# Kernel optimization log

Measured on AMD Instinct MI355X. Metric: run time of the kernel, lower is better.

The kernel has to match this reference:

```python
import jax, jax.numpy as jnp
import numpy as np

B, S, D = 2, 2048, 1024
N_HEADS, D_HEAD = 16, 64
INIT_STD = 0.02


def setup_inputs() -> dict:
    key = jax.random.key(0)
    k_res, k_q, k_k, k_v, k_o = jax.random.split(key, 5)
    residual = jax.random.normal(k_res, (B, S, D), dtype=jnp.float32)
    W_Q = INIT_STD * jax.random.normal(k_q, (N_HEADS, D_HEAD, D), dtype=jnp.float32)
    W_K = INIT_STD * jax.random.normal(k_k, (N_HEADS, D_HEAD, D), dtype=jnp.float32)
    W_V = INIT_STD * jax.random.normal(k_v, (N_HEADS, D_HEAD, D), dtype=jnp.float32)
    W_O = INIT_STD * jax.random.normal(k_o, (N_HEADS, D_HEAD, D), dtype=jnp.float32)
    return {"residual": residual, "W_Q": W_Q, "W_K": W_K, "W_V": W_V, "W_O": W_O}


def reference(residual, W_Q, W_K, W_V, W_O):
    seq_len = residual.shape[1]
    # projections: [b, n, p, h]  (heads first, matching q.transpose(1,2))
    q = jnp.einsum('bpd,nhd->bnph', residual, W_Q)
    k = jnp.einsum('bpd,nhd->bnph', residual, W_K)
    v = jnp.einsum('bpd,nhd->bnph', residual, W_V)
    scale = 1.0 / jnp.sqrt(jnp.asarray(q.shape[-1], dtype=residual.dtype))
    # [b, n, p_q, p_k] full score matrix (faithful to original naive impl)
    scores = jnp.einsum('bnqh,bnkh->bnqk', q, k) * scale
    causal = jnp.tril(jnp.ones((seq_len, seq_len), dtype=bool))
    scores = jnp.where(causal, scores, -jnp.inf)
    pattern = jax.nn.softmax(scores, axis=-1)
    attn_out = jnp.einsum('bnqk,bnkh->bnqh', pattern, v)
    # output projection summed over heads: 'bpnh,nhd->bpd'
    return jnp.einsum('bnph,nhd->bpd', attn_out, W_O)
```

## Files before the change

### kernel.cpp

```cpp
#include <hip/hip_runtime.h>
#include <math.h>


#define SS_ 2048
#define DD_ 1024
#define NH_ 16
#define BN_ 32
#define BS_ 4096

typedef __bf16 bf16x8 __attribute__((ext_vector_type(8)));
typedef __bf16 bf16x4 __attribute__((ext_vector_type(4)));
typedef short shortx4 __attribute__((ext_vector_type(4)));
typedef float floatx4 __attribute__((ext_vector_type(4)));
typedef unsigned short ushortx4 __attribute__((ext_vector_type(4)));

__device__ __forceinline__ unsigned short f2bf(float f) {
    union { float f; unsigned u; } v; v.f = f;
    unsigned r = v.u + 0x7FFFu + ((v.u >> 16) & 1u);
    return (unsigned short)(r >> 16);
}

__device__ __forceinline__ floatx4 mfma_pv(bf16x4 a, bf16x4 b, floatx4 c) {
#if __has_builtin(__builtin_amdgcn_mfma_f32_16x16x16_bf16)
    return __builtin_amdgcn_mfma_f32_16x16x16_bf16(a, b, c, 0, 0, 0);
#else
    return __builtin_amdgcn_mfma_f32_16x16x16bf16_1k(
        __builtin_bit_cast(shortx4, a), __builtin_bit_cast(shortx4, b), c, 0, 0, 0);
#endif
}

__device__ __forceinline__ void gl_lds16(const unsigned short* g, unsigned short* l) {
    __builtin_amdgcn_global_load_lds(
        (const __attribute__((address_space(1))) unsigned int*)g,
        (__attribute__((address_space(3))) unsigned int*)l, 16, 0, 0);
}

__global__ __launch_bounds__(256) void cast_bf16_kernel(
    const float* __restrict__ resid, const float* __restrict__ WQ,
    const float* __restrict__ WK, const float* __restrict__ WV,
    unsigned short* __restrict__ residB, unsigned short* __restrict__ WQb,
    unsigned short* __restrict__ WKb, unsigned short* __restrict__ WVb)
{
    const int z = blockIdx.y;
    if (z > 0 && blockIdx.x >= 1024) return;
    const float* src = (z == 0) ? resid : (z == 1) ? WQ : (z == 2) ? WK : WV;
    unsigned short* dst = (z == 0) ? residB : (z == 1) ? WQb : (z == 2) ? WKb : WVb;
    const int i = (blockIdx.x * 256 + threadIdx.x) * 4;
    float4 f = *(const float4*)(src + i);
    ushortx4 o;
    o[0] = f2bf(f.x); o[1] = f2bf(f.y); o[2] = f2bf(f.z); o[3] = f2bf(f.w);
    *(ushortx4*)(dst + i) = o;
}

__global__ __launch_bounds__(256) void wo_transpose_kernel(
    const float* __restrict__ WO, unsigned short* __restrict__ WOt)
{
    __shared__ float t[64][65];
    const int kk0 = blockIdx.x * 64, d0 = blockIdx.y * 64;
    #pragma unroll
    for (int it = 0; it < 16; ++it) {
        int idx = it * 256 + threadIdx.x;
        int r = idx >> 6, c = idx & 63;
        t[r][c] = WO[(kk0 + r) * DD_ + d0 + c];
    }
    __syncthreads();
    #pragma unroll
    for (int it = 0; it < 16; ++it) {
        int idx = it * 256 + threadIdx.x;
        int r = idx >> 6, c = idx & 63;
        WOt[(d0 + r) * DD_ + kk0 + c] = f2bf(t[c][r]);
    }
}

__global__ __launch_bounds__(256) void qkv_m97_kernel(
    const unsigned short* __restrict__ residB,
    const unsigned short* __restrict__ WQb,
    const unsigned short* __restrict__ WKb,
    const unsigned short* __restrict__ WVb,
    unsigned short* __restrict__ q, unsigned short* __restrict__ kk,
    unsigned short* __restrict__ vT)
{
    __shared__ unsigned short As[128 * 64];
    __shared__ unsigned short Bs[128 * 64];
    const int tid = threadIdx.x;
    const int l = tid & 63, w = tid >> 6;
    const int quad = l >> 4, lan = l & 15;
    const int z = blockIdx.z;
    const unsigned short* W = (z == 0) ? WQb : (z == 1) ? WKb : WVb;
    unsigned short* dst = (z == 0) ? q : (z == 1) ? kk : vT;
    const int mBase = blockIdx.x * 128;
    const int nBase = blockIdx.y * 128;
    const int wm = (w & 1) * 64, wn = (w >> 1) * 64;

    floatx4 acc[4][4];
    #pragma unroll
    for (int a = 0; a < 4; ++a)
        #pragma unroll
        for (int b = 0; b < 4; ++b)
            #pragma unroll
            for (int i = 0; i < 4; ++i) acc[a][b][i] = 0.f;

    const int sr = l >> 3;
    const int sgx = ((l & 7) ^ sr) * 8;
    const int sw = (l & 7) ^ (lan & 7);

    for (int k0 = 0; k0 < DD_; k0 += 64) {
        __syncthreads();
        #pragma unroll
        for (int i = 0; i < 4; ++i) {
            const int row = i * 32 + w * 8 + sr;
            gl_lds16(residB + (size_t)(mBase + row) * DD_ + k0 + sgx,
                     As + i * 2048 + w * 512);
            gl_lds16(W + (size_t)(nBase + row) * DD_ + k0 + sgx,
                     Bs + i * 2048 + w * 512);
        }
        __syncthreads();
        #pragma unroll
        for (int ks = 0; ks < 2; ++ks) {
            const int fo = (((ks * 4 + quad) ^ (lan & 7)) << 3);
            bf16x8 a[4], b[4];
            #pragma unroll
            for (int mi = 0; mi < 4; ++mi)
                a[mi] = *(const bf16x8*)(As + (wm + mi * 16 + lan) * 64 + fo);
            #pragma unroll
            for (int ni = 0; ni < 4; ++ni)
                b[ni] = *(const bf16x8*)(Bs + (wn + ni * 16 + lan) * 64 + fo);
            #pragma unroll
            for (int mi = 0; mi < 4; ++mi)
                #pragma unroll
                for (int ni = 0; ni < 4; ++ni)
                    acc[mi][ni] = __builtin_amdgcn_mfma_f32_16x16x32_bf16(
                        a[mi], b[ni], acc[mi][ni], 0, 0, 0);
        }
    }
    const int headU = (nBase + wn) >> 6;
    const float scale = (z == 0) ? 0.125f * 1.44269504088896340736f : 1.0f;
    if (z < 2) {
        #pragma unroll
        for (int mi = 0; mi < 4; ++mi)
            #pragma unroll
            for (int ni = 0; ni < 4; ++ni)
                #pragma unroll
                for (int reg = 0; reg < 4; ++reg) {
                    int m = mBase + wm + mi * 16 + quad * 4 + reg;
                    int bb = m >> 11, ss = m & 2047;
                    int h = ni * 16 + lan;
                    dst[((size_t)(bb * NH_ + headU) * SS_ + ss) * 64 + h] =
                        f2bf(acc[mi][ni][reg] * scale);
                }
    } else {
        #pragma unroll
        for (int mi = 0; mi < 4; ++mi) {
            const int m0 = mBase + wm + mi * 16 + quad * 4;
            const int bb = m0 >> 11, ss0 = m0 & 2047;
            #pragma unroll
            for (int ni = 0; ni < 4; ++ni) {
                const int h = ni * 16 + lan;
                bf16x4 ob;
                #pragma unroll
                for (int reg = 0; reg < 4; ++reg)
                    ob[reg] = static_cast<__bf16>(acc[mi][ni][reg]);
                *(bf16x4*)(dst + ((size_t)(bb * NH_ + headU) * 64 + h) * SS_ + ss0) = ob;
            }
        }
    }
}

__global__ __launch_bounds__(256) void flash_mfma_kernel(
    const unsigned short* __restrict__ q,
    const unsigned short* __restrict__ k,
    const unsigned short* __restrict__ vT,
    unsigned short* __restrict__ attn)
{
    __shared__ unsigned short ldsK[2][64 * 64];
    __shared__ unsigned short ldsV[2][64 * 64];
    const int l = threadIdx.x & 63, w = threadIdx.x >> 6;
    const int quad = l >> 4, lan = l & 15;
    const int f = blockIdx.x;
    const int bn = (f & 7) | (((f >> 3) & 3) << 3);
    const int p = f >> 5;

    const unsigned short* Qg = q  + (size_t)bn * SS_ * 64;
    const unsigned short* Kg = k  + (size_t)bn * SS_ * 64;
    const unsigned short* Vg = vT + (size_t)bn * 64 * SS_;

    const int srl = l >> 3;
    const int sgx = (l & 7) ^ srl;

    #pragma unroll
    for (int half = 0; half < 2; ++half) {
        const int chunk = (half == 0) ? p : 31 - p;
        const int qRow0 = chunk * 64 + w * 16;
        const int qAbs = qRow0 + lan;

        const unsigned short* Qr = Qg + (size_t)qAbs * 64 + quad * 8;
        bf16x8 Qf0 = *(const bf16x8*)(Qr);
        bf16x8 Qf1 = *(const bf16x8*)(Qr + 32);

        float mrow = -INFINITY, lrow = 0.f;
        floatx4 o[4];
        #pragma unroll
        for (int t = 0; t < 4; ++t)
            #pragma unroll
            for (int i = 0; i < 4; ++i) o[t][i] = 0.f;

        __syncthreads();
        #pragma unroll
        for (int i = 0; i < 2; ++i) {
            const int row = w * 16 + i * 8;
            gl_lds16(Kg + (size_t)(row + srl) * 64 + sgx * 8, &ldsK[0][row * 64]);
            gl_lds16(Vg + (size_t)(row + srl) * SS_ + sgx * 8, &ldsV[0][row * 64]);
        }

        for (int kt = 0; kt <= chunk; ++kt) {
            const int kBase = kt * 64;
            const int buf = kt & 1;
            __syncthreads();
            if (kt < chunk) {
                const int kB1 = kBase + 64;
                #pragma unroll
                for (int i = 0; i < 2; ++i) {
                    const int row = w * 16 + i * 8;
                    gl_lds16(Kg + (size_t)(kB1 + row + srl) * 64 + sgx * 8,
                             &ldsK[buf ^ 1][row * 64]);
                    gl_lds16(Vg + (size_t)(row + srl) * SS_ + kB1 + sgx * 8,
                             &ldsV[buf ^ 1][row * 64]);
                }
            }
            const unsigned short* Kb = &ldsK[buf][0];
            const unsigned short* Vb = &ldsV[buf][0];

            floatx4 sc[4];
            #pragma unroll
            for (int nt = 0; nt < 4; ++nt) {
                const unsigned short* kr = Kb + (nt * 16 + lan) * 64;
                bf16x8 K0 = *(const bf16x8*)(kr + ((quad ^ (lan & 7)) << 3));
                bf16x8 K1 = *(const bf16x8*)(kr + (((quad + 4) ^ (lan & 7)) << 3));
                floatx4 zz; zz[0] = zz[1] = zz[2] = zz[3] = 0.f;
                sc[nt] = __builtin_amdgcn_mfma_f32_16x16x32_bf16(K0, Qf0, zz, 0, 0, 0);
                sc[nt] = __builtin_amdgcn_mfma_f32_16x16x32_bf16(K1, Qf1, sc[nt], 0, 0, 0);
            }
            if (kt == chunk) {
                #pragma unroll
                for (int nt = 0; nt < 4; ++nt)
                    #pragma unroll
                    for (int reg = 0; reg < 4; ++reg)
                        if (kBase + nt * 16 + quad * 4 + reg > qAbs)
                            sc[nt][reg] = -INFINITY;
            }
            float mx = sc[0][0];
            #pragma unroll
            for (int nt = 0; nt < 4; ++nt)
                #pragma unroll
                for (int reg = 0; reg < 4; ++reg) mx = fmaxf(mx, sc[nt][reg]);
            mx = fmaxf(mx, __shfl_xor(mx, 16, 64));
            mx = fmaxf(mx, __shfl_xor(mx, 32, 64));
            const float mnew = fmaxf(mrow, mx);
            const float alpha = exp2f(mrow - mnew);
            bf16x4 pb[4];
            float sum = 0.f;
            #pragma unroll
            for (int nt = 0; nt < 4; ++nt)
                #pragma unroll
                for (int reg = 0; reg < 4; ++reg) {
                    float pp = exp2f(sc[nt][reg] - mnew);
                    sum += pp;
                    pb[nt][reg] = static_cast<__bf16>(pp);
                }
            sum += __shfl_xor(sum, 16, 64);
            sum += __shfl_xor(sum, 32, 64);
            lrow = lrow * alpha + sum;
            mrow = mnew;
            #pragma unroll
            for (int t = 0; t < 4; ++t)
                #pragma unroll
                for (int i = 0; i < 4; ++i) o[t][i] *= alpha;
            #pragma unroll
            for (int t = 0; t < 4; ++t) {
                const unsigned short* vr = Vb + (t * 16 + lan) * 64 + ((quad & 1) << 2);
                #pragma unroll
                for (int nt = 0; nt < 4; ++nt) {
                    const int g = nt * 2 + (quad >> 1);
                    bf16x4 Vf = *(const bf16x4*)(vr + ((g ^ (lan & 7)) << 3));
                    o[t] = mfma_pv(Vf, pb[nt], o[t]);
                }
            }
        }
        const float rl = 1.f / lrow;
        #pragma unroll
        for (int t = 0; t < 4; ++t) {
            bf16x4 ob;
            #pragma unroll
            for (int reg = 0; reg < 4; ++reg)
                ob[reg] = static_cast<__bf16>(o[t][reg] * rl);
            *(bf16x4*)(attn + ((size_t)bn * SS_ + qAbs) * 64 + t * 16 + quad * 4) = ob;
        }
    }
}

__global__ __launch_bounds__(256) void out_m97_kernel(
    const unsigned short* __restrict__ attn,
    const unsigned short* __restrict__ WOt,
    float* __restrict__ out)
{
    __shared__ unsigned short As[128 * 64];
    __shared__ unsigned short Bs[128 * 64];
    const int tid = threadIdx.x;
    const int l = tid & 63, w = tid >> 6;
    const int quad = l >> 4, lan = l & 15;
    const int mBase = blockIdx.x * 128;
    const int nBase = blockIdx.y * 128;
    const int wm = (w & 1) * 64, wn = (w >> 1) * 64;
    const int bbU = mBase >> 11;
    const int ssBase = mBase & 2047;

    floatx4 acc[4][4];
    #pragma unroll
    for (int a = 0; a < 4; ++a)
        #pragma unroll
        for (int b = 0; b < 4; ++b)
            #pragma unroll
            for (int i = 0; i < 4; ++i) acc[a][b][i] = 0.f;

    const int sr = l >> 3;
    const int sgx = ((l & 7) ^ sr) * 8;

    for (int kt = 0; kt < 16; ++kt) {
        const int k0 = kt * 64;
        __syncthreads();
        #pragma unroll
        for (int i = 0; i < 4; ++i) {
            const int row = i * 32 + w * 8 + sr;
            gl_lds16(attn + ((size_t)(bbU * NH_ + kt) * SS_ + ssBase + row) * 64 + sgx,
                     As + i * 2048 + w * 512);
            gl_lds16(WOt + (size_t)(nBase + row) * DD_ + k0 + sgx,
                     Bs + i * 2048 + w * 512);
        }
        __syncthreads();
        #pragma unroll
        for (int ks = 0; ks < 2; ++ks) {
            const int fo = (((ks * 4 + quad) ^ (lan & 7)) << 3);
            bf16x8 a[4], b[4];
            #pragma unroll
            for (int mi = 0; mi < 4; ++mi)
                a[mi] = *(const bf16x8*)(As + (wm + mi * 16 + lan) * 64 + fo);
            #pragma unroll
            for (int ni = 0; ni < 4; ++ni)
                b[ni] = *(const bf16x8*)(Bs + (wn + ni * 16 + lan) * 64 + fo);
            #pragma unroll
            for (int mi = 0; mi < 4; ++mi)
                #pragma unroll
                for (int ni = 0; ni < 4; ++ni)
                    acc[mi][ni] = __builtin_amdgcn_mfma_f32_16x16x32_bf16(
                        a[mi], b[ni], acc[mi][ni], 0, 0, 0);
        }
    }
    #pragma unroll
    for (int mi = 0; mi < 4; ++mi)
        #pragma unroll
        for (int ni = 0; ni < 4; ++ni)
            #pragma unroll
            for (int reg = 0; reg < 4; ++reg) {
                int m = mBase + wm + mi * 16 + quad * 4 + reg;
                out[(size_t)m * DD_ + nBase + wn + ni * 16 + lan] = acc[mi][ni][reg];
            }
}

extern "C" void kernel_launch(void* const* d_in, const int* in_sizes, int n_in,
                              void* d_out, int out_size, void* d_ws, size_t ws_size,
                              hipStream_t stream) {
    const float* resid = (const float*)d_in[0];
    const float* WQ    = (const float*)d_in[1];
    const float* WK    = (const float*)d_in[2];
    const float* WV    = (const float*)d_in[3];
    const float* WO    = (const float*)d_in[4];
    float* out = (float*)d_out;

    unsigned short* q      = (unsigned short*)d_ws;
    unsigned short* kk     = q      + 4194304;
    unsigned short* vT     = kk     + 4194304;
    unsigned short* attn   = vT     + 4194304;
    unsigned short* residB = attn   + 4194304;
    unsigned short* WQb    = residB + 4194304;
    unsigned short* WKb    = WQb    + 1048576;
    unsigned short* WVb    = WKb    + 1048576;
    unsigned short* WOt    = WVb    + 1048576;

    cast_bf16_kernel<<<dim3(4096, 4), 256, 0, stream>>>(
        resid, WQ, WK, WV, residB, WQb, WKb, WVb);
    wo_transpose_kernel<<<dim3(16, 16), 256, 0, stream>>>(WO, WOt);
    qkv_m97_kernel<<<dim3(32, 8, 3), 256, 0, stream>>>(
        residB, WQb, WKb, WVb, q, kk, vT);
    flash_mfma_kernel<<<dim3(512), dim3(256), 0, stream>>>(q, kk, vT, attn);
    out_m97_kernel<<<dim3(32, 8), 256, 0, stream>>>(attn, WOt, out);
}
```

Measured before the change: 206.1 us.

## Split flash blocks to one query chunk each and compute row sums via MFMA

The flash attention kernel now launches 1024 blocks, each handling a single 64-row query chunk, ordered longest-first. Previously 512 blocks each paired a short and a long chunk. The softmax denominator is now accumulated with an MFMA against a ones vector instead of scalar adds plus cross-lane shuffles. This exposes more parallelism and removes the shuffle reductions, at the cost of extra MFMA work and possible tail imbalance. It also drops an unused variable in the QKV kernel.

```diff
diff --git a/kernel.cpp b/kernel.cpp
--- a/kernel.cpp
+++ b/kernel.cpp
@@ -102,7 +102,6 @@
 
     const int sr = l >> 3;
     const int sgx = ((l & 7) ^ sr) * 8;
-    const int sw = (l & 7) ^ (lan & 7);
 
     for (int k0 = 0; k0 < DD_; k0 += 64) {
         __syncthreads();
@@ -178,7 +177,7 @@
     const int quad = l >> 4, lan = l & 15;
     const int f = blockIdx.x;
     const int bn = (f & 7) | (((f >> 3) & 3) << 3);
-    const int p = f >> 5;
+    const int chunk = 31 - (f >> 5);
 
     const unsigned short* Qg = q  + (size_t)bn * SS_ * 64;
     const unsigned short* Kg = k  + (size_t)bn * SS_ * 64;
@@ -187,114 +186,113 @@
     const int srl = l >> 3;
     const int sgx = (l & 7) ^ srl;
 
-    #pragma unroll
-    for (int half = 0; half < 2; ++half) {
-        const int chunk = (half == 0) ? p : 31 - p;
-        const int qRow0 = chunk * 64 + w * 16;
-        const int qAbs = qRow0 + lan;
-
-        const unsigned short* Qr = Qg + (size_t)qAbs * 64 + quad * 8;
-        bf16x8 Qf0 = *(const bf16x8*)(Qr);
-        bf16x8 Qf1 = *(const bf16x8*)(Qr + 32);
-
-        float mrow = -INFINITY, lrow = 0.f;
-        floatx4 o[4];
+    const int qRow0 = chunk * 64 + w * 16;
+    const int qAbs = qRow0 + lan;
+
+    const unsigned short* Qr = Qg + (size_t)qAbs * 64 + quad * 8;
+    bf16x8 Qf0 = *(const bf16x8*)(Qr);
+    bf16x8 Qf1 = *(const bf16x8*)(Qr + 32);
+
+    bf16x4 ones;
+    #pragma unroll
+    for (int i = 0; i < 4; ++i) ones[i] = static_cast<__bf16>(1.0f);
+
+    float mrow = -INFINITY;
+    floatx4 l_acc;
+    floatx4 o[4];
+    #pragma unroll
+    for (int i = 0; i < 4; ++i) l_acc[i] = 0.f;
+    #pragma unroll
+    for (int t = 0; t < 4; ++t)
+        #pragma unroll
+        for (int i = 0; i < 4; ++i) o[t][i] = 0.f;
+
+    #pragma unroll
+    for (int i = 0; i < 2; ++i) {
+        const int row = w * 16 + i * 8;
+        gl_lds16(Kg + (size_t)(row + srl) * 64 + sgx * 8, &ldsK[0][row * 64]);
+        gl_lds16(Vg + (size_t)(row + srl) * SS_ + sgx * 8, &ldsV[0][row * 64]);
+    }
+
+    for (int kt = 0; kt <= chunk; ++kt) {
+        const int kBase = kt * 64;
+        const int buf = kt & 1;
+        __syncthreads();
+        if (kt < chunk) {
+            const int kB1 = kBase + 64;
+            #pragma unroll
+            for (int i = 0; i < 2; ++i) {
+                const int row = w * 16 + i * 8;
+                gl_lds16(Kg + (size_t)(kB1 + row + srl) * 64 + sgx * 8,
+                         &ldsK[buf ^ 1][row * 64]);
+                gl_lds16(Vg + (size_t)(row + srl) * SS_ + kB1 + sgx * 8,
+                         &ldsV[buf ^ 1][row * 64]);
+            }
+        }
+        const unsigned short* Kb = &ldsK[buf][0];
+        const unsigned short* Vb = &ldsV[buf][0];
+
+        floatx4 sc[4];
+        #pragma unroll
+        for (int nt = 0; nt < 4; ++nt) {
+            const unsigned short* kr = Kb + (nt * 16 + lan) * 64;
+            bf16x8 K0 = *(const bf16x8*)(kr + ((quad ^ (lan & 7)) << 3));
+            bf16x8 K1 = *(const bf16x8*)(kr + (((quad + 4) ^ (lan & 7)) << 3));
+            floatx4 zz; zz[0] = zz[1] = zz[2] = zz[3] = 0.f;
+            sc[nt] = __builtin_amdgcn_mfma_f32_16x16x32_bf16(K0, Qf0, zz, 0, 0, 0);
+            sc[nt] = __builtin_amdgcn_mfma_f32_16x16x32_bf16(K1, Qf1, sc[nt], 0, 0, 0);
+        }
+        if (kt == chunk) {
+            #pragma unroll
+            for (int nt = 0; nt < 4; ++nt)
+                #pragma unroll
+                for (int reg = 0; reg < 4; ++reg)
+                    if (kBase + nt * 16 + quad * 4 + reg > qAbs)
+                        sc[nt][reg] = -INFINITY;
+        }
+        float mx = sc[0][0];
+        #pragma unroll
+        for (int nt = 0; nt < 4; ++nt)
+            #pragma unroll
+            for (int reg = 0; reg < 4; ++reg) mx = fmaxf(mx, sc[nt][reg]);
+        mx = fmaxf(mx, __shfl_xor(mx, 16, 64));
+        mx = fmaxf(mx, __shfl_xor(mx, 32, 64));
+        const float mnew = fmaxf(mrow, mx);
+        const float alpha = exp2f(mrow - mnew);
+        mrow = mnew;
+        bf16x4 pb[4];
+        #pragma unroll
+        for (int nt = 0; nt < 4; ++nt)
+            #pragma unroll
+            for (int reg = 0; reg < 4; ++reg)
+                pb[nt][reg] = static_cast<__bf16>(exp2f(sc[nt][reg] - mnew));
+        l_acc[0] *= alpha;
         #pragma unroll
         for (int t = 0; t < 4; ++t)
             #pragma unroll
-            for (int i = 0; i < 4; ++i) o[t][i] = 0.f;
-
-        __syncthreads();
-        #pragma unroll
-        for (int i = 0; i < 2; ++i) {
-            const int row = w * 16 + i * 8;
-            gl_lds16(Kg + (size_t)(row + srl) * 64 + sgx * 8, &ldsK[0][row * 64]);
-            gl_lds16(Vg + (size_t)(row + srl) * SS_ + sgx * 8, &ldsV[0][row * 64]);
-        }
-
-        for (int kt = 0; kt <= chunk; ++kt) {
-            const int kBase = kt * 64;
-            const int buf = kt & 1;
-            __syncthreads();
-            if (kt < chunk) {
-                const int kB1 = kBase + 64;
-                #pragma unroll
-                for (int i = 0; i < 2; ++i) {
-                    const int row = w * 16 + i * 8;
-                    gl_lds16(Kg + (size_t)(kB1 + row + srl) * 64 + sgx * 8,
-                             &ldsK[buf ^ 1][row * 64]);
-                    gl_lds16(Vg + (size_t)(row + srl) * SS_ + kB1 + sgx * 8,
-                             &ldsV[buf ^ 1][row * 64]);
-                }
+            for (int i = 0; i < 4; ++i) o[t][i] *= alpha;
+        #pragma unroll
+        for (int nt = 0; nt < 4; ++nt)
+            l_acc = mfma_pv(ones, pb[nt], l_acc);
+        #pragma unroll
+        for (int t = 0; t < 4; ++t) {
+            const unsigned short* vr = Vb + (t * 16 + lan) * 64 + ((quad & 1) << 2);
+            #pragma unroll
+            for (int nt = 0; nt < 4; ++nt) {
+                const int g = nt * 2 + (quad >> 1);
+                bf16x4 Vf = *(const bf16x4*)(vr + ((g ^ (lan & 7)) << 3));
+                o[t] = mfma_pv(Vf, pb[nt], o[t]);
             }
-            const unsigned short* Kb = &ldsK[buf][0];
-            const unsigned short* Vb = &ldsV[buf][0];
-
-            floatx4 sc[4];
-            #pragma unroll
-            for (int nt = 0; nt < 4; ++nt) {
-                const unsigned short* kr = Kb + (nt * 16 + lan) * 64;
-                bf16x8 K0 = *(const bf16x8*)(kr + ((quad ^ (lan & 7)) << 3));
-                bf16x8 K1 = *(const bf16x8*)(kr + (((quad + 4) ^ (lan & 7)) << 3));
-                floatx4 zz; zz[0] = zz[1] = zz[2] = zz[3] = 0.f;
-                sc[nt] = __builtin_amdgcn_mfma_f32_16x16x32_bf16(K0, Qf0, zz, 0, 0, 0);
-                sc[nt] = __builtin_amdgcn_mfma_f32_16x16x32_bf16(K1, Qf1, sc[nt], 0, 0, 0);
-            }
-            if (kt == chunk) {
-                #pragma unroll
-                for (int nt = 0; nt < 4; ++nt)
-                    #pragma unroll
-                    for (int reg = 0; reg < 4; ++reg)
-                        if (kBase + nt * 16 + quad * 4 + reg > qAbs)
-                            sc[nt][reg] = -INFINITY;
-            }
-            float mx = sc[0][0];
-            #pragma unroll
-            for (int nt = 0; nt < 4; ++nt)
-                #pragma unroll
-                for (int reg = 0; reg < 4; ++reg) mx = fmaxf(mx, sc[nt][reg]);
-            mx = fmaxf(mx, __shfl_xor(mx, 16, 64));
-            mx = fmaxf(mx, __shfl_xor(mx, 32, 64));
-            const float mnew = fmaxf(mrow, mx);
-            const float alpha = exp2f(mrow - mnew);
-            bf16x4 pb[4];
-            float sum = 0.f;
-            #pragma unroll
-            for (int nt = 0; nt < 4; ++nt)
-                #pragma unroll
-                for (int reg = 0; reg < 4; ++reg) {
-                    float pp = exp2f(sc[nt][reg] - mnew);
-                    sum += pp;
-                    pb[nt][reg] = static_cast<__bf16>(pp);
-                }
-            sum += __shfl_xor(sum, 16, 64);
-            sum += __shfl_xor(sum, 32, 64);
-            lrow = lrow * alpha + sum;
-            mrow = mnew;
-            #pragma unroll
-            for (int t = 0; t < 4; ++t)
-                #pragma unroll
-                for (int i = 0; i < 4; ++i) o[t][i] *= alpha;
-            #pragma unroll
-            for (int t = 0; t < 4; ++t) {
-                const unsigned short* vr = Vb + (t * 16 + lan) * 64 + ((quad & 1) << 2);
-                #pragma unroll
-                for (int nt = 0; nt < 4; ++nt) {
-                    const int g = nt * 2 + (quad >> 1);
-                    bf16x4 Vf = *(const bf16x4*)(vr + ((g ^ (lan & 7)) << 3));
-                    o[t] = mfma_pv(Vf, pb[nt], o[t]);
-                }
-            }
-        }
-        const float rl = 1.f / lrow;
-        #pragma unroll
-        for (int t = 0; t < 4; ++t) {
-            bf16x4 ob;
-            #pragma unroll
-            for (int reg = 0; reg < 4; ++reg)
-                ob[reg] = static_cast<__bf16>(o[t][reg] * rl);
-            *(bf16x4*)(attn + ((size_t)bn * SS_ + qAbs) * 64 + t * 16 + quad * 4) = ob;
-        }
+        }
+    }
+    const float rl = 1.f / l_acc[0];
+    #pragma unroll
+    for (int t = 0; t < 4; ++t) {
+        bf16x4 ob;
+        #pragma unroll
+        for (int reg = 0; reg < 4; ++reg)
+            ob[reg] = static_cast<__bf16>(o[t][reg] * rl);
+        *(bf16x4*)(attn + ((size_t)bn * SS_ + qAbs) * 64 + t * 16 + quad * 4) = ob;
     }
 }
 
@@ -391,6 +389,6 @@
     wo_transpose_kernel<<<dim3(16, 16), 256, 0, stream>>>(WO, WOt);
     qkv_m97_kernel<<<dim3(32, 8, 3), 256, 0, stream>>>(
         residB, WQb, WKb, WVb, q, kk, vT);
-    flash_mfma_kernel<<<dim3(512), dim3(256), 0, stream>>>(q, kk, vT, attn);
+    flash_mfma_kernel<<<dim3(1024), dim3(256), 0, stream>>>(q, kk, vT, attn);
     out_m97_kernel<<<dim3(32, 8), 256, 0, stream>>>(attn, WOt, out);
 }
```

Result: faster. 196.7 us (-4.6%).
